# Optimization experiments

Hardware: AMD Instinct MI355X
Metric: run time of the kernel (lower is better)

The kernel has to match this reference:

```python
import jax, jax.numpy as jnp
import numpy as np

B, N, M = 8, 8192, 2048
C, CP = 256, 256          # num_features, num_features_prev
D1, D2 = 256, 256         # layer_dims
BN_EPS = 1e-5


def setup_inputs() -> dict:
    key = jax.random.key(0)
    ks = jax.random.split(key, 8)
    return {
        "xyz": jax.random.normal(ks[0], (B, N, 3), dtype=jnp.float32),
        "xyz_prev": jax.random.normal(ks[1], (B, M, 3), dtype=jnp.float32),
        "features": jax.random.normal(ks[2], (B, C, N), dtype=jnp.float32),
        "features_prev": jax.random.normal(ks[3], (B, CP, M), dtype=jnp.float32),
        "w1": jax.random.normal(ks[4], (D1, C + CP), dtype=jnp.float32) * 0.02,
        "b1": jnp.zeros((D1,), dtype=jnp.float32),
        "g1": jnp.ones((D1,), dtype=jnp.float32),
        "beta1": jnp.zeros((D1,), dtype=jnp.float32),
        "w2": jax.random.normal(ks[5], (D2, D1), dtype=jnp.float32) * 0.02,
        "b2": jnp.zeros((D2,), dtype=jnp.float32),
        "g2": jnp.ones((D2,), dtype=jnp.float32),
        "beta2": jnp.zeros((D2,), dtype=jnp.float32),
    }


def _three_nn(unknown, known):
    # squared pairwise distances via GEMM form: [B, n, m]
    sq_u = jnp.sum(unknown * unknown, axis=-1)          # [B, n]
    sq_k = jnp.sum(known * known, axis=-1)              # [B, m]
    d2 = sq_u[:, :, None] + sq_k[:, None, :] - 2.0 * jnp.einsum(
        "bnd,bmd->bnm", unknown, known)
    neg_top, idx = jax.lax.top_k(-d2, 3)                # 3 smallest, ascending
    dist = jnp.sqrt(jnp.maximum(-neg_top, 0.0))         # [B, n, 3]
    return dist, idx


def _three_interpolate(features, idx, weight):
    # features [B, c, m], idx [B, n, 3], weight [B, n, 3] -> [B, c, n]
    gathered = jax.vmap(lambda f, i: f[:, i])(features, idx)  # [B, c, n, 3]
    return jnp.einsum("bcnk,bnk->bcn", gathered, weight)


def _bn_relu(x, gamma, beta):
    # training-mode BatchNorm1d over (batch, points), biased variance
    mean = jnp.mean(x, axis=(0, 2), keepdims=True)
    var = jnp.var(x, axis=(0, 2), keepdims=True)
    xh = (x - mean) * jax.lax.rsqrt(var + BN_EPS)
    return jnp.maximum(xh * gamma[None, :, None] + beta[None, :, None], 0.0)


def reference(xyz, xyz_prev, features, features_prev,
              w1, b1, g1, beta1, w2, b2, g2, beta2):
    dist, idx = _three_nn(xyz, xyz_prev)
    inv = 1.0 / (dist + 1e-8)
    weights = inv / jnp.sum(inv, axis=2, keepdims=True)           # [B, n, 3]
    new_features = _three_interpolate(features_prev, idx, weights)  # [B, cp, n]
    x = jnp.concatenate([new_features, features], axis=1)           # [B, cp+c, n]
    x = _bn_relu(jnp.einsum("oi,bin->bon", w1, x) + b1[None, :, None], g1, beta1)
    x = _bn_relu(jnp.einsum("oi,bin->bon", w2, x) + b2[None, :, None], g2, beta2)
    return x
```

## Files before the change

kernel.cpp:

```cpp
#include <hip/hip_runtime.h>

#define BDIM 8
#define NPTS 8192
#define MPTS 2048
#define NCHUNK 8
#define CHSZ 256
#define NSAMP 65536.0f
#define PITCH 40

typedef __attribute__((ext_vector_type(8))) short bf16x8;
typedef __attribute__((ext_vector_type(4))) float f32x4;

static __device__ __forceinline__ unsigned short f2bf(float f) {
  unsigned int x = __float_as_uint(f);
  x += 0x7FFFu + ((x >> 16) & 1u);
  return (unsigned short)(x >> 16);
}
static __device__ __forceinline__ float bf2f(unsigned short u) {
  return __uint_as_float(((unsigned int)u) << 16);
}

__global__ __launch_bounds__(256)
void three_nn_part_kernel(const float* __restrict__ xyz, const float* __restrict__ xyz_prev,
                          float4* __restrict__ pd, int4* __restrict__ pi) {
  __shared__ __align__(16) float4 pk[CHSZ];
  const int tid = threadIdx.x;
  const int ch = blockIdx.y, b = blockIdx.z;
  const int mbase = ch*CHSZ;
  {
    const int j = mbase + tid;
    float x = xyz_prev[((size_t)b*MPTS + j)*3 + 0];
    float y = xyz_prev[((size_t)b*MPTS + j)*3 + 1];
    float z = xyz_prev[((size_t)b*MPTS + j)*3 + 2];
    float s = __fadd_rn(__fadd_rn(__fmul_rn(x,x), __fmul_rn(y,y)), __fmul_rn(z,z));
    pk[tid] = make_float4(x, y, z, s);
  }
  __syncthreads();
  const int n = blockIdx.x*256 + tid;
  const size_t qoff = ((size_t)b*NPTS + n)*3;
  const float qx = xyz[qoff], qy = xyz[qoff+1], qz = xyz[qoff+2];
  const float squ = __fadd_rn(__fadd_rn(__fmul_rn(qx,qx), __fmul_rn(qy,qy)), __fmul_rn(qz,qz));

  float d0 = 3.4e38f, d1 = 3.4e38f, d2v = 3.4e38f;
  int j0 = 0, j1 = 0, j2 = 0;
  for (int m = 0; m < CHSZ; m += 16) {
    float dd[16];
    #pragma unroll
    for (int u = 0; u < 16; ++u) {
      const float4 p = pk[m + u];
      float dot = __fadd_rn(__fadd_rn(__fmul_rn(qx,p.x), __fmul_rn(qy,p.y)), __fmul_rn(qz,p.z));
      dd[u] = __fsub_rn(__fadd_rn(squ, p.w), __fmul_rn(2.0f, dot));
    }
    float mn = dd[0];
    #pragma unroll
    for (int u = 1; u < 16; ++u) mn = fminf(mn, dd[u]);
    if (mn < d2v) {
      #pragma unroll
      for (int u = 0; u < 16; ++u) {
        const float v = dd[u];
        if (v < d2v) {
          if (v < d1) {
            d2v = d1; j2 = j1;
            if (v < d0) { d1 = d0; j1 = j0; d0 = v; j0 = mbase + m + u; }
            else        { d1 = v;  j1 = mbase + m + u; }
          } else { d2v = v; j2 = mbase + m + u; }
        }
      }
    }
  }
  const size_t q = (size_t)b*NPTS + n;
  pd[(size_t)ch*(BDIM*NPTS) + q] = make_float4(d0, d1, d2v, 0.f);
  pi[(size_t)ch*(BDIM*NPTS) + q] = make_int4(j0, j1, j2, 0);
}

__global__ __launch_bounds__(256)
void nn_merge_kernel(const float4* __restrict__ pd, const int4* __restrict__ pi,
                     int* __restrict__ idx_out, float* __restrict__ wgt_out) {
  const size_t q = (size_t)blockIdx.x*256 + threadIdx.x;
  float d0 = 3.4e38f, d1 = 3.4e38f, d2v = 3.4e38f;
  int j0 = 0, j1 = 0, j2 = 0;
  #pragma unroll
  for (int c = 0; c < NCHUNK; ++c) {
    const float4 dv = pd[(size_t)c*(BDIM*NPTS) + q];
    const int4   iv = pi[(size_t)c*(BDIM*NPTS) + q];
    const float dl[3] = {dv.x, dv.y, dv.z};
    const int   jl[3] = {iv.x, iv.y, iv.z};
    #pragma unroll
    for (int t = 0; t < 3; ++t) {
      const float v = dl[t]; const int j = jl[t];
      if (v < d2v) {
        if (v < d1) {
          d2v = d1; j2 = j1;
          if (v < d0) { d1 = d0; j1 = j0; d0 = v; j0 = j; }
          else        { d1 = v;  j1 = j; }
        } else { d2v = v; j2 = j; }
      }
    }
  }
  const float s0 = sqrtf(fmaxf(d0, 0.f));
  const float s1 = sqrtf(fmaxf(d1, 0.f));
  const float s2 = sqrtf(fmaxf(d2v, 0.f));
  const float i0 = 1.f/(s0 + 1e-8f), i1 = 1.f/(s1 + 1e-8f), i2 = 1.f/(s2 + 1e-8f);
  const float sum = i0 + i1 + i2;
  idx_out[q*3] = j0; idx_out[q*3+1] = j1; idx_out[q*3+2] = j2;
  wgt_out[q*3] = i0/sum; wgt_out[q*3+1] = i1/sum; wgt_out[q*3+2] = i2/sum;
}

__global__ __launch_bounds__(256)
void cvt2_kernel(const float* __restrict__ w1, const float* __restrict__ w2,
                 unsigned short* __restrict__ d1, unsigned short* __restrict__ d2) {
  int t = blockIdx.x*256 + threadIdx.x;
  if (t < 131072) d1[t] = f2bf(w1[t]);
  else            d2[t - 131072] = f2bf(w2[t - 131072]);
}

template<int SRCW, int DPITCH, int DOFF>
__global__ __launch_bounds__(256)
void trans_bf16_kernel(const float* __restrict__ src, unsigned short* __restrict__ dst) {
  __shared__ __align__(16) unsigned short St[64][72];
  const int tid = threadIdx.x;
  const int n0 = blockIdx.x*64, c0 = blockIdx.y*64, b = blockIdx.z;
  const int cl = tid >> 2;
  #pragma unroll
  for (int i = 0; i < 4; ++i) {
    int nl = (tid & 3)*16 + i*4;
    float4 v = *(const float4*)&src[((size_t)(b*256 + c0 + cl))*SRCW + n0 + nl];
    St[cl][nl]   = f2bf(v.x); St[cl][nl+1] = f2bf(v.y);
    St[cl][nl+2] = f2bf(v.z); St[cl][nl+3] = f2bf(v.w);
  }
  __syncthreads();
  #pragma unroll
  for (int i = 0; i < 2; ++i) {
    int u = tid + i*256;
    int nl = u >> 3, c8 = (u & 7)*8;
    unsigned short tmp[8];
    #pragma unroll
    for (int j = 0; j < 8; ++j) tmp[j] = St[c8 + j][nl];
    *(uint4*)&dst[((size_t)(b*SRCW + n0 + nl))*DPITCH + DOFF + c0 + c8] = *(uint4*)tmp;
  }
}

__global__ __launch_bounds__(256)
void interp_t_kernel(const unsigned short* __restrict__ fpT, const int* __restrict__ idx,
                     const float* __restrict__ wgt, unsigned short* __restrict__ X1t) {
  const int tid = threadIdx.x;
  const int b = blockIdx.y;
  const int n = blockIdx.x*8 + (tid >> 5);
  const int c8 = (tid & 31)*8;
  const size_t p = ((size_t)b*NPTS + n)*3;
  const int i0 = idx[p], i1 = idx[p+1], i2 = idx[p+2];
  const float w0 = wgt[p], w1 = wgt[p+1], w2 = wgt[p+2];
  const unsigned short* fb = fpT + (size_t)b*MPTS*256 + c8;
  uint4 a0 = *(const uint4*)&fb[(size_t)i0*256];
  uint4 a1 = *(const uint4*)&fb[(size_t)i1*256];
  uint4 a2 = *(const uint4*)&fb[(size_t)i2*256];
  const unsigned short* u0 = (const unsigned short*)&a0;
  const unsigned short* u1 = (const unsigned short*)&a1;
  const unsigned short* u2 = (const unsigned short*)&a2;
  unsigned short r[8];
  #pragma unroll
  for (int j = 0; j < 8; ++j) {
    float v = bf2f(u0[j])*w0 + bf2f(u1[j])*w1 + bf2f(u2[j])*w2;
    r[j] = f2bf(v);
  }
  *(uint4*)&X1t[((size_t)b*NPTS + n)*512 + c8] = *(uint4*)r;
}

template<int KD, int MODE>
__global__ __launch_bounds__(512)
void gemm_t_kernel(const unsigned short* __restrict__ W, const unsigned short* __restrict__ X,
                   const float* __restrict__ bias, const float* __restrict__ scl,
                   const float* __restrict__ shf, unsigned short* __restrict__ Y,
                   float* __restrict__ part) {
  __shared__ __align__(16) unsigned short Ws[256*PITCH];
  __shared__ __align__(16) unsigned short Xs[128*PITCH];
  __shared__ float lsum[256], lsq[256];
  const int tid = threadIdx.x;
  const int b = blockIdx.y, n0 = blockIdx.x*128;
  const int row = tid >> 2, seg = tid & 3;
  const unsigned short* Xb = X + (size_t)(b*NPTS + n0)*KD;

  if (tid < 256) { lsum[tid] = 0.f; lsq[tid] = 0.f; }

  uint4 wv0 = *(const uint4*)&W[(size_t)row*KD + seg*8];
  uint4 wv1 = *(const uint4*)&W[(size_t)(row+128)*KD + seg*8];
  uint4 xv  = *(const uint4*)&Xb[(size_t)row*KD + seg*8];

  f32x4 acc[4][4];
  #pragma unroll
  for (int i = 0; i < 4; ++i)
    #pragma unroll
    for (int j = 0; j < 4; ++j) acc[i][j] = (f32x4){0.f,0.f,0.f,0.f};

  const int lane = tid & 63, l16 = lane & 15, quad = lane >> 4;
  const int wave = tid >> 6, wo = wave >> 1, wn = wave & 1;

  for (int kt = 0; kt < KD/32; ++kt) {
    __syncthreads();
    *(uint4*)&Ws[row*PITCH + seg*8]       = wv0;
    *(uint4*)&Ws[(row+128)*PITCH + seg*8] = wv1;
    if (MODE == 0) {
      *(uint4*)&Xs[row*PITCH + seg*8] = xv;
    } else {
      const int kc = kt*32 + seg*8;
      float4 s0 = *(const float4*)&scl[kc], s1 = *(const float4*)&scl[kc+4];
      float4 h0 = *(const float4*)&shf[kc], h1 = *(const float4*)&shf[kc+4];
      const unsigned short* xu = (const unsigned short*)&xv;
      unsigned short t[8];
      t[0] = f2bf(fmaxf(fmaf(bf2f(xu[0]), s0.x, h0.x), 0.f));
      t[1] = f2bf(fmaxf(fmaf(bf2f(xu[1]), s0.y, h0.y), 0.f));
      t[2] = f2bf(fmaxf(fmaf(bf2f(xu[2]), s0.z, h0.z), 0.f));
      t[3] = f2bf(fmaxf(fmaf(bf2f(xu[3]), s0.w, h0.w), 0.f));
      t[4] = f2bf(fmaxf(fmaf(bf2f(xu[4]), s1.x, h1.x), 0.f));
      t[5] = f2bf(fmaxf(fmaf(bf2f(xu[5]), s1.y, h1.y), 0.f));
      t[6] = f2bf(fmaxf(fmaf(bf2f(xu[6]), s1.z, h1.z), 0.f));
      t[7] = f2bf(fmaxf(fmaf(bf2f(xu[7]), s1.w, h1.w), 0.f));
      *(uint4*)&Xs[row*PITCH + seg*8] = *(uint4*)t;
    }
    __syncthreads();
    if (kt + 1 < KD/32) {
      const int k0 = (kt+1)*32;
      wv0 = *(const uint4*)&W[(size_t)row*KD + k0 + seg*8];
      wv1 = *(const uint4*)&W[(size_t)(row+128)*KD + k0 + seg*8];
      xv  = *(const uint4*)&Xb[(size_t)row*KD + k0 + seg*8];
    }
    bf16x8 af[4], bfr[4];
    #pragma unroll
    for (int to = 0; to < 4; ++to)
      af[to] = *(const bf16x8*)&Ws[(wo*64 + to*16 + l16)*PITCH + quad*8];
    #pragma unroll
    for (int tn = 0; tn < 4; ++tn)
      bfr[tn] = *(const bf16x8*)&Xs[(wn*64 + tn*16 + l16)*PITCH + quad*8];
    #pragma unroll
    for (int to = 0; to < 4; ++to)
      #pragma unroll
      for (int tn = 0; tn < 4; ++tn)
        acc[to][tn] = __builtin_amdgcn_mfma_f32_16x16x32_bf16(af[to], bfr[tn], acc[to][tn], 0, 0, 0);
  }

  #pragma unroll
  for (int to = 0; to < 4; ++to) {
    #pragma unroll
    for (int r = 0; r < 4; ++r) {
      const int o = wo*64 + to*16 + quad*4 + r;
      const float bv = bias[o];
      float p = 0.f, q = 0.f;
      #pragma unroll
      for (int tn = 0; tn < 4; ++tn) {
        float v = acc[to][tn][r] + bv;
        acc[to][tn][r] = v;
        p += v; q = fmaf(v, v, q);
      }
      #pragma unroll
      for (int m = 1; m < 16; m <<= 1) { p += __shfl_xor(p, m); q += __shfl_xor(q, m); }
      if (l16 == 0) { atomicAdd(&lsum[o], p); atomicAdd(&lsq[o], q); }
    }
  }
  #pragma unroll
  for (int to = 0; to < 4; ++to)
    #pragma unroll
    for (int tn = 0; tn < 4; ++tn) {
      const int n = n0 + wn*64 + tn*16 + l16;
      const int o = wo*64 + to*16 + quad*4;
      unsigned int lo = (unsigned)f2bf(acc[to][tn][0]) | ((unsigned)f2bf(acc[to][tn][1]) << 16);
      unsigned int hi = (unsigned)f2bf(acc[to][tn][2]) | ((unsigned)f2bf(acc[to][tn][3]) << 16);
      *(uint2*)&Y[((size_t)(b*NPTS + n))*256 + o] = make_uint2(lo, hi);
    }
  __syncthreads();
  if (tid < 256) {
    const int blk = b*gridDim.x + blockIdx.x;
    part[(size_t)blk*512 + tid]       = lsum[tid];
    part[(size_t)blk*512 + 256 + tid] = lsq[tid];
  }
}

__global__ __launch_bounds__(256)
void bn_reduce_kernel(const float* __restrict__ part, const float* __restrict__ g,
                      const float* __restrict__ beta, float* __restrict__ scl,
                      float* __restrict__ shf) {
  __shared__ float ls[4], lq[4];
  const int o = blockIdx.x;
  const int t = threadIdx.x;
  float s = part[(size_t)t*512 + o]        + part[(size_t)(t+256)*512 + o];
  float q = part[(size_t)t*512 + 256 + o]  + part[(size_t)(t+256)*512 + 256 + o];
  #pragma unroll
  for (int m = 1; m < 64; m <<= 1) { s += __shfl_xor(s, m); q += __shfl_xor(q, m); }
  const int w = t >> 6;
  if ((t & 63) == 0) { ls[w] = s; lq[w] = q; }
  __syncthreads();
  if (t == 0) {
    const float ss = ls[0] + ls[1] + ls[2] + ls[3];
    const float qq = lq[0] + lq[1] + lq[2] + lq[3];
    const float inv_n = 1.0f / NSAMP;
    const float mean = ss * inv_n;
    const float var  = qq * inv_n - mean*mean;
    const float sc = g[o] * rsqrtf(var + 1e-5f);
    scl[o] = sc;
    shf[o] = beta[o] - mean * sc;
  }
}

__global__ __launch_bounds__(256)
void bn2_t_kernel(const unsigned short* __restrict__ Yt, const float* __restrict__ scl,
                  const float* __restrict__ shf, float* __restrict__ out) {
  __shared__ __align__(16) unsigned short T[64][72];
  const int tid = threadIdx.x;
  const int n0 = blockIdx.x*64, o0 = blockIdx.y*64, b = blockIdx.z;
  #pragma unroll
  for (int i = 0; i < 2; ++i) {
    int u = tid + i*256;
    int nl = u >> 3, o8 = (u & 7)*8;
    uint4 v = *(const uint4*)&Yt[((size_t)(b*NPTS + n0 + nl))*256 + o0 + o8];
    *(uint4*)&T[nl][o8] = v;
  }
  __syncthreads();
  #pragma unroll
  for (int i = 0; i < 4; ++i) {
    int u = tid + i*256;
    int ol = u >> 4, n4 = (u & 15)*4;
    const float s = scl[o0+ol], h = shf[o0+ol];
    float4 v;
    v.x = fmaxf(fmaf(bf2f(T[n4  ][ol]), s, h), 0.f);
    v.y = fmaxf(fmaf(bf2f(T[n4+1][ol]), s, h), 0.f);
    v.z = fmaxf(fmaf(bf2f(T[n4+2][ol]), s, h), 0.f);
    v.w = fmaxf(fmaf(bf2f(T[n4+3][ol]), s, h), 0.f);
    *(float4*)&out[((size_t)(b*256 + o0 + ol))*NPTS + n0 + n4] = v;
  }
}

extern "C" void kernel_launch(void* const* d_in, const int* in_sizes, int n_in,
                              void* d_out, int out_size, void* d_ws, size_t ws_size,
                              hipStream_t stream) {
  const float* xyz           = (const float*)d_in[0];
  const float* xyz_prev      = (const float*)d_in[1];
  const float* features      = (const float*)d_in[2];
  const float* features_prev = (const float*)d_in[3];
  const float* w1    = (const float*)d_in[4];
  const float* b1    = (const float*)d_in[5];
  const float* g1    = (const float*)d_in[6];
  const float* beta1 = (const float*)d_in[7];
  const float* w2    = (const float*)d_in[8];
  const float* b2    = (const float*)d_in[9];
  const float* g2    = (const float*)d_in[10];
  const float* beta2 = (const float*)d_in[11];
  float* out = (float*)d_out;

  char* ws = (char*)d_ws;
  int*            idxb = (int*)ws;
  float*          wgtb = (float*)(ws + 786432);
  float*          bn   = (float*)(ws + 1572864);
  unsigned short* w1b  = (unsigned short*)(ws + 1581056);
  unsigned short* w2b  = (unsigned short*)(ws + 1843200);
  unsigned short* X1t  = (unsigned short*)(ws + 2097152);
  unsigned short* y2t  = X1t;
  unsigned short* y1t  = (unsigned short*)d_out;
  unsigned short* fpT  = (unsigned short*)((char*)d_out + 33554432);
  float*          part = (float*)((char*)d_out + 41943040);
  float4*         pd   = (float4*)((char*)d_out + 46137344);
  int4*           pi   = (int4*)((char*)d_out + 54525952);

  float* bn1_scl = bn;        float* bn1_shf = bn + 256;
  float* bn2_scl = bn + 512;  float* bn2_shf = bn + 768;

  cvt2_kernel<<<768, 256, 0, stream>>>(w1, w2, w1b, w2b);

  three_nn_part_kernel<<<dim3(NPTS/256, NCHUNK, BDIM), 256, 0, stream>>>(xyz, xyz_prev, pd, pi);
  nn_merge_kernel<<<(BDIM*NPTS)/256, 256, 0, stream>>>(pd, pi, idxb, wgtb);

  trans_bf16_kernel<NPTS, 512, 256><<<dim3(NPTS/64, 4, BDIM), 256, 0, stream>>>(features, X1t);
  trans_bf16_kernel<MPTS, 256, 0><<<dim3(MPTS/64, 4, BDIM), 256, 0, stream>>>(features_prev, fpT);

  interp_t_kernel<<<dim3(NPTS/8, BDIM), 256, 0, stream>>>(fpT, idxb, wgtb, X1t);

  gemm_t_kernel<512, 0><<<dim3(NPTS/128, BDIM), 512, 0, stream>>>(
      w1b, X1t, b1, nullptr, nullptr, y1t, part);
  bn_reduce_kernel<<<256, 256, 0, stream>>>(part, g1, beta1, bn1_scl, bn1_shf);

  gemm_t_kernel<256, 1><<<dim3(NPTS/128, BDIM), 512, 0, stream>>>(
      w2b, y1t, b2, bn1_scl, bn1_shf, y2t, part);
  bn_reduce_kernel<<<256, 256, 0, stream>>>(part, g2, beta2, bn2_scl, bn2_shf);

  bn2_t_kernel<<<dim3(NPTS/64, 4, BDIM), 256, 0, stream>>>(y2t, bn2_scl, bn2_shf, out);
}
```

Before: 315.4 us.

## Fuse three-point interpolation gather into first GEMM's operand load

Drops the separate interpolation kernel and the interleaved 512-wide X1t buffer. The first GEMM now gathers the three neighbour rows from the transposed previous features, blends them with the weights in registers for the first 256 K-columns, and reads the transposed current features for the remaining 256. This saves one full write and read of the interpolated half of the activation matrix and one kernel launch. The cost is that gathers, which may scatter across memory, now sit in the GEMM's K-loop prefetch, so load latency may be less hidden.

```diff
diff --git a/kernel.cpp b/kernel.cpp
--- a/kernel.cpp
+++ b/kernel.cpp
@@ -140,30 +140,130 @@
   }
 }
 
-__global__ __launch_bounds__(256)
-void interp_t_kernel(const unsigned short* __restrict__ fpT, const int* __restrict__ idx,
-                     const float* __restrict__ wgt, unsigned short* __restrict__ X1t) {
+__global__ __launch_bounds__(512)
+void gemm1_fused_kernel(const unsigned short* __restrict__ W,
+                        const unsigned short* __restrict__ Xf,
+                        const unsigned short* __restrict__ fpT,
+                        const int* __restrict__ idx, const float* __restrict__ wgt,
+                        const float* __restrict__ bias,
+                        unsigned short* __restrict__ Y, float* __restrict__ part) {
+  __shared__ __align__(16) unsigned short Ws[256*PITCH];
+  __shared__ __align__(16) unsigned short Xs[128*PITCH];
+  __shared__ float lsum[256], lsq[256];
   const int tid = threadIdx.x;
-  const int b = blockIdx.y;
-  const int n = blockIdx.x*8 + (tid >> 5);
-  const int c8 = (tid & 31)*8;
-  const size_t p = ((size_t)b*NPTS + n)*3;
-  const int i0 = idx[p], i1 = idx[p+1], i2 = idx[p+2];
-  const float w0 = wgt[p], w1 = wgt[p+1], w2 = wgt[p+2];
-  const unsigned short* fb = fpT + (size_t)b*MPTS*256 + c8;
-  uint4 a0 = *(const uint4*)&fb[(size_t)i0*256];
-  uint4 a1 = *(const uint4*)&fb[(size_t)i1*256];
-  uint4 a2 = *(const uint4*)&fb[(size_t)i2*256];
-  const unsigned short* u0 = (const unsigned short*)&a0;
-  const unsigned short* u1 = (const unsigned short*)&a1;
-  const unsigned short* u2 = (const unsigned short*)&a2;
-  unsigned short r[8];
-  #pragma unroll
-  for (int j = 0; j < 8; ++j) {
-    float v = bf2f(u0[j])*w0 + bf2f(u1[j])*w1 + bf2f(u2[j])*w2;
-    r[j] = f2bf(v);
-  }
-  *(uint4*)&X1t[((size_t)b*NPTS + n)*512 + c8] = *(uint4*)r;
+  const int b = blockIdx.y, n0 = blockIdx.x*128;
+  const int row = tid >> 2, seg = tid & 3;
+
+  if (tid < 256) { lsum[tid] = 0.f; lsq[tid] = 0.f; }
+
+  const size_t p = ((size_t)b*NPTS + n0 + row)*3;
+  const int   i0 = idx[p],  i1 = idx[p+1],  i2 = idx[p+2];
+  const float w0 = wgt[p],  w1 = wgt[p+1],  w2 = wgt[p+2];
+  const unsigned short* fb  = fpT + (size_t)b*MPTS*256;
+  const unsigned short* Xfb = Xf  + ((size_t)(b*NPTS + n0) + row)*256;
+
+  uint4 wv0 = *(const uint4*)&W[(size_t)row*512 + seg*8];
+  uint4 wv1 = *(const uint4*)&W[(size_t)(row+128)*512 + seg*8];
+  uint4 xv;
+  {
+    const int k0 = seg*8;
+    uint4 a0 = *(const uint4*)&fb[(size_t)i0*256 + k0];
+    uint4 a1 = *(const uint4*)&fb[(size_t)i1*256 + k0];
+    uint4 a2 = *(const uint4*)&fb[(size_t)i2*256 + k0];
+    const unsigned short* u0 = (const unsigned short*)&a0;
+    const unsigned short* u1 = (const unsigned short*)&a1;
+    const unsigned short* u2 = (const unsigned short*)&a2;
+    unsigned short r[8];
+    #pragma unroll
+    for (int j = 0; j < 8; ++j)
+      r[j] = f2bf(bf2f(u0[j])*w0 + bf2f(u1[j])*w1 + bf2f(u2[j])*w2);
+    xv = *(uint4*)r;
+  }
+
+  f32x4 acc[4][4];
+  #pragma unroll
+  for (int i = 0; i < 4; ++i)
+    #pragma unroll
+    for (int j = 0; j < 4; ++j) acc[i][j] = (f32x4){0.f,0.f,0.f,0.f};
+
+  const int lane = tid & 63, l16 = lane & 15, quad = lane >> 4;
+  const int wave = tid >> 6, wo = wave >> 1, wn = wave & 1;
+
+  for (int kt = 0; kt < 16; ++kt) {
+    __syncthreads();
+    *(uint4*)&Ws[row*PITCH + seg*8]       = wv0;
+    *(uint4*)&Ws[(row+128)*PITCH + seg*8] = wv1;
+    *(uint4*)&Xs[row*PITCH + seg*8]       = xv;
+    __syncthreads();
+    if (kt + 1 < 16) {
+      const int k0 = (kt+1)*32;
+      wv0 = *(const uint4*)&W[(size_t)row*512 + k0 + seg*8];
+      wv1 = *(const uint4*)&W[(size_t)(row+128)*512 + k0 + seg*8];
+      const int kx = k0 + seg*8;
+      if (kx < 256) {
+        uint4 a0 = *(const uint4*)&fb[(size_t)i0*256 + kx];
+        uint4 a1 = *(const uint4*)&fb[(size_t)i1*256 + kx];
+        uint4 a2 = *(const uint4*)&fb[(size_t)i2*256 + kx];
+        const unsigned short* u0 = (const unsigned short*)&a0;
+        const unsigned short* u1 = (const unsigned short*)&a1;
+        const unsigned short* u2 = (const unsigned short*)&a2;
+        unsigned short r[8];
+        #pragma unroll
+        for (int j = 0; j < 8; ++j)
+          r[j] = f2bf(bf2f(u0[j])*w0 + bf2f(u1[j])*w1 + bf2f(u2[j])*w2);
+        xv = *(uint4*)r;
+      } else {
+        xv = *(const uint4*)&Xfb[kx - 256];
+      }
+    }
+    bf16x8 af[4], bfr[4];
+    #pragma unroll
+    for (int to = 0; to < 4; ++to)
+      af[to] = *(const bf16x8*)&Ws[(wo*64 + to*16 + l16)*PITCH + quad*8];
+    #pragma unroll
+    for (int tn = 0; tn < 4; ++tn)
+      bfr[tn] = *(const bf16x8*)&Xs[(wn*64 + tn*16 + l16)*PITCH + quad*8];
+    #pragma unroll
+    for (int to = 0; to < 4; ++to)
+      #pragma unroll
+      for (int tn = 0; tn < 4; ++tn)
+        acc[to][tn] = __builtin_amdgcn_mfma_f32_16x16x32_bf16(af[to], bfr[tn], acc[to][tn], 0, 0, 0);
+  }
+
+  #pragma unroll
+  for (int to = 0; to < 4; ++to) {
+    #pragma unroll
+    for (int r = 0; r < 4; ++r) {
+      const int o = wo*64 + to*16 + quad*4 + r;
+      const float bv = bias[o];
+      float ps = 0.f, qs = 0.f;
+      #pragma unroll
+      for (int tn = 0; tn < 4; ++tn) {
+        float v = acc[to][tn][r] + bv;
+        acc[to][tn][r] = v;
+        ps += v; qs = fmaf(v, v, qs);
+      }
+      #pragma unroll
+      for (int m = 1; m < 16; m <<= 1) { ps += __shfl_xor(ps, m); qs += __shfl_xor(qs, m); }
+      if (l16 == 0) { atomicAdd(&lsum[o], ps); atomicAdd(&lsq[o], qs); }
+    }
+  }
+  #pragma unroll
+  for (int to = 0; to < 4; ++to)
+    #pragma unroll
+    for (int tn = 0; tn < 4; ++tn) {
+      const int n = n0 + wn*64 + tn*16 + l16;
+      const int o = wo*64 + to*16 + quad*4;
+      unsigned int lo = (unsigned)f2bf(acc[to][tn][0]) | ((unsigned)f2bf(acc[to][tn][1]) << 16);
+      unsigned int hi = (unsigned)f2bf(acc[to][tn][2]) | ((unsigned)f2bf(acc[to][tn][3]) << 16);
+      *(uint2*)&Y[((size_t)(b*NPTS + n))*256 + o] = make_uint2(lo, hi);
+    }
+  __syncthreads();
+  if (tid < 256) {
+    const int blk = b*gridDim.x + blockIdx.x;
+    part[(size_t)blk*512 + tid]       = lsum[tid];
+    part[(size_t)blk*512 + 256 + tid] = lsq[tid];
+  }
 }
 
 template<int KD, int MODE>
@@ -351,8 +451,8 @@
   float*          bn   = (float*)(ws + 1572864);
   unsigned short* w1b  = (unsigned short*)(ws + 1581056);
   unsigned short* w2b  = (unsigned short*)(ws + 1843200);
-  unsigned short* X1t  = (unsigned short*)(ws + 2097152);
-  unsigned short* y2t  = X1t;
+  unsigned short* Xf   = (unsigned short*)(ws + 2097152);
+  unsigned short* y2t  = Xf;
   unsigned short* y1t  = (unsigned short*)d_out;
   unsigned short* fpT  = (unsigned short*)((char*)d_out + 33554432);
   float*          part = (float*)((char*)d_out + 41943040);
@@ -367,13 +467,11 @@
   three_nn_part_kernel<<<dim3(NPTS/256, NCHUNK, BDIM), 256, 0, stream>>>(xyz, xyz_prev, pd, pi);
   nn_merge_kernel<<<(BDIM*NPTS)/256, 256, 0, stream>>>(pd, pi, idxb, wgtb);
 
-  trans_bf16_kernel<NPTS, 512, 256><<<dim3(NPTS/64, 4, BDIM), 256, 0, stream>>>(features, X1t);
+  trans_bf16_kernel<NPTS, 256, 0><<<dim3(NPTS/64, 4, BDIM), 256, 0, stream>>>(features, Xf);
   trans_bf16_kernel<MPTS, 256, 0><<<dim3(MPTS/64, 4, BDIM), 256, 0, stream>>>(features_prev, fpT);
 
-  interp_t_kernel<<<dim3(NPTS/8, BDIM), 256, 0, stream>>>(fpT, idxb, wgtb, X1t);
-
-  gemm_t_kernel<512, 0><<<dim3(NPTS/128, BDIM), 512, 0, stream>>>(
-      w1b, X1t, b1, nullptr, nullptr, y1t, part);
+  gemm1_fused_kernel<<<dim3(NPTS/128, BDIM), 512, 0, stream>>>(
+      w1b, Xf, fpT, idxb, wgtb, b1, y1t, part);
   bn_reduce_kernel<<<256, 256, 0, stream>>>(part, g1, beta1, bn1_scl, bn1_shf);
 
   gemm_t_kernel<256, 1><<<dim3(NPTS/128, BDIM), 512, 0, stream>>>(
```

New measurement: 305.8 us. -3.0%, faster.
